# Optimization experiments

Hardware: AMD Instinct MI355X
Metric: run time of the kernel (lower is better)

The kernel has to match this reference:

```python
import jax, jax.numpy as jnp
import numpy as np

WIN = (8, 8)
N_WIN_TOK = WIN[0] * WIN[1]  # 64
DIM = 128
HEADS = 4
HEAD_DIM = DIM // HEADS
HIDDEN = int(DIM * 0.25)
B_ = 16384


def _relative_position_index():
    ch = np.arange(WIN[0])
    cw = np.arange(WIN[1])
    coords = np.stack(np.meshgrid(ch, cw, indexing='ij'))      # (2, Wh, Ww)
    flat = coords.reshape(2, -1)                                # (2, N)
    rel = flat[:, :, None] - flat[:, None, :]                   # (2, N, N)
    rel = rel.transpose(1, 2, 0).astype(np.int32)               # (N, N, 2)
    rel[:, :, 0] += WIN[0] - 1
    rel[:, :, 1] += WIN[1] - 1
    rel[:, :, 0] *= 2 * WIN[1] - 1
    return jnp.asarray(rel.sum(-1), dtype=jnp.int32)            # (N, N)


def setup_inputs() -> dict:
    key = jax.random.key(0)
    ks = jax.random.split(key, 8)
    s_in = 1.0 / np.sqrt(DIM)
    s_h = 1.0 / np.sqrt(HIDDEN)
    return {
        'x': jax.random.normal(ks[0], (B_, N_WIN_TOK, DIM), jnp.float32),
        'rpb_table': 0.02 * jax.random.normal(ks[1], ((2 * WIN[0] - 1) * (2 * WIN[1] - 1), HEADS), jnp.float32),
        'wq': s_in * jax.random.normal(ks[2], (DIM, DIM), jnp.float32),
        'bq': jnp.zeros((DIM,), jnp.float32),
        'wkv': s_in * jax.random.normal(ks[3], (DIM, 2 * DIM), jnp.float32),
        'bkv': jnp.zeros((2 * DIM,), jnp.float32),
        'fc1_w': s_in * jax.random.normal(ks[4], (DIM, HIDDEN), jnp.float32),
        'fc1_b': jnp.zeros((HIDDEN,), jnp.float32),
        'fc2_w': s_h * jax.random.normal(ks[5], (HIDDEN, DIM), jnp.float32),
        'fc2_b': jnp.zeros((DIM,), jnp.float32),
        'rel_idx': _relative_position_index(),
    }


def reference(x, rpb_table, wq, bq, wkv, bkv, fc1_w, fc1_b, fc2_w, fc2_b, rel_idx):
    B, N, C = x.shape
    scale = HEAD_DIM ** -0.5
    # qkv projections (Uformer LinearProjection): q from to_q, k/v from to_kv
    q = (x @ wq + bq).reshape(B, N, HEADS, HEAD_DIM).transpose(0, 2, 1, 3)   # (B,h,N,d)
    kv = (x @ wkv + bkv).reshape(B, N, 2, HEADS, HEAD_DIM)
    k = kv[:, :, 0].transpose(0, 2, 1, 3)                                    # (B,h,N,d)
    v = kv[:, :, 1].transpose(0, 2, 1, 3)
    attn = jnp.einsum('bhnd,bhmd->bhnm', q * scale, k)                       # (B,h,N,N)
    bias = rpb_table[rel_idx]                                                # (N,N,h)
    attn = attn + bias.transpose(2, 0, 1)[None]                              # + (1,h,N,N)
    attn = jax.nn.softmax(attn, axis=-1)
    out = jnp.einsum('bhnm,bhmd->bhnd', attn, v).transpose(0, 2, 1, 3).reshape(B, N, C)
    # Mlp proj: fc1 -> GELU -> fc2
    out = jax.nn.gelu(out @ fc1_w + fc1_b, approximate=False) @ fc2_w + fc2_b
    return out
```

## Files before the change

### kernel.cpp

```cpp
#include <hip/hip_runtime.h>
#include <hip/hip_bf16.h>
#include <math.h>

typedef __bf16 bf16x8 __attribute__((ext_vector_type(8)));
typedef __bf16 bf16x4 __attribute__((ext_vector_type(4)));
typedef float f32x4 __attribute__((ext_vector_type(4)));

static __device__ __forceinline__ f32x4 mfma16(bf16x8 a, bf16x8 b, f32x4 c) {
  return __builtin_amdgcn_mfma_f32_16x16x32_bf16(a, b, c, 0, 0, 0);
}


__global__ void wattn_prep(const float* __restrict__ wq, const float* __restrict__ bq,
                           const float* __restrict__ wkv,
                           const float* __restrict__ f1w, const float* __restrict__ f2w,
                           const float* __restrict__ rpb, const int* __restrict__ rel,
                           char* __restrict__ ws)
{
  const int idx = blockIdx.x * 256 + threadIdx.x;
  const float scale = 0.17677669529663687f;
  unsigned short* ws16 = (unsigned short*)ws;
  float* wsf = (float*)ws;

  if (idx < 2048) {
    const int lane = idx & 63, dt = (idx >> 6) & 7, kt = idx >> 9;
    const int gg = lane >> 4, cc = lane & 15;
    bf16x8 v;
#pragma unroll
    for (int i = 0; i < 8; ++i)
      v[i] = (__bf16)(wq[(kt * 32 + gg * 8 + i) * 128 + dt * 16 + cc] * scale);
    *(bf16x8*)(ws16 + idx * 8) = v;
  } else if (idx < 4096) {
    const int e = idx - 2048;
    const int lane = e & 63, dt = (e >> 6) & 7, kt = e >> 9;
    const int gg = lane >> 4, cc = lane & 15;
    bf16x8 v;
#pragma unroll
    for (int i = 0; i < 8; ++i)
      v[i] = (__bf16)(wkv[(kt * 32 + gg * 8 + i) * 256 + dt * 16 + cc]);
    *(bf16x8*)(ws16 + 16384 + e * 8) = v;
  } else if (idx < 6144) {
    const int e = idx - 4096;
    const int lane = e & 63, dt = (e >> 6) & 7, kt = e >> 9;
    const int gg = lane >> 4, cc = lane & 15;
    bf16x8 v;
#pragma unroll
    for (int i = 0; i < 8; ++i)
      v[i] = (__bf16)(wkv[(kt * 32 + gg * 8 + i) * 256 + 128 + dt * 16 + cc]);
    *(bf16x8*)(ws16 + 32768 + e * 8) = v;
  } else if (idx < 6656) {
    const int e = idx - 6144;
    const int lane = e & 63, ht = (e >> 6) & 1, kt = e >> 7;
    const int gg = lane >> 4, cc = lane & 15;
    bf16x8 v;
#pragma unroll
    for (int i = 0; i < 8; ++i)
      v[i] = (__bf16)(f1w[(kt * 32 + gg * 8 + i) * 32 + ht * 16 + cc]);
    *(bf16x8*)(ws16 + 49152 + e * 8) = v;
  } else if (idx < 7168) {
    const int e = idx - 6656;
    const int lane = e & 63, dt = e >> 6;
    const int gg = lane >> 4, cc = lane & 15;
    bf16x8 v;
#pragma unroll
    for (int i = 0; i < 8; ++i)
      v[i] = (__bf16)(f2w[(gg * 8 + i) * 128 + dt * 16 + cc]);
    *(bf16x8*)(ws16 + 53248 + e * 8) = v;
  } else if (idx < 11264) {
    const int e = idx - 7168;
    const int lane = e & 63, nt = (e >> 6) & 3, mt = (e >> 8) & 3, h = e >> 10;
    const int gg = lane >> 4, cc = lane & 15;
    const int q = nt * 16 + cc;
    f32x4 v;
#pragma unroll
    for (int r = 0; r < 4; ++r) {
      const int key = mt * 16 + gg * 4 + r;
      v[r] = rpb[rel[q * 64 + key] * 4 + h];
    }
    *(f32x4*)(wsf + 28672 + e * 4) = v;
  } else if (idx < 11392) {
    const int d = idx - 11264;
    wsf[45056 + d] = bq[d] * scale;
  }
}

__global__ __launch_bounds__(256, 3) void wattn_main(
    const float* __restrict__ x,
    const float* __restrict__ bkv,
    const float* __restrict__ f1b,
    const float* __restrict__ f2b,
    const char* __restrict__ ws,
    float* __restrict__ out)
{
  extern __shared__ char smem[];
  const int tid = threadIdx.x;
  const int w = tid >> 6;
  const int l = tid & 63;
  const int g = l >> 4;
  const int c = l & 15;
  const size_t b = blockIdx.x;
  const int WB = w * 12288;
  const int QB = WB, KB = WB + 4096, VB = WB + 8192;
  const int PB = WB, OB = WB + 8192, HB = WB;

  const unsigned short* ws16 = (const unsigned short*)ws;
  const bf16x8* wqp = (const bf16x8*)(ws16);
  const bf16x8* wkp = (const bf16x8*)(ws16 + 16384);
  const bf16x8* wvp = (const bf16x8*)(ws16 + 32768);
  const bf16x8* f1p = (const bf16x8*)(ws16 + 49152);
  const bf16x8* f2p = (const bf16x8*)(ws16 + 53248);
  const f32x4* biasp = (const f32x4*)(ws16 + 57344);
  const float* bqs = (const float*)(ws16 + 90112);

  bf16x8 xf[4][4];
  {
    const float* xg = x + b * 8192;
#pragma unroll
    for (int tt = 0; tt < 4; ++tt)
#pragma unroll
      for (int kt = 0; kt < 4; ++kt) {
        const float* p = xg + (tt * 16 + c) * 128 + kt * 32 + g * 8;
        f32x4 u = *(const f32x4*)p;
        f32x4 v = *(const f32x4*)(p + 4);
        bf16x8 f = { (__bf16)u[0], (__bf16)u[1], (__bf16)u[2], (__bf16)u[3],
                     (__bf16)v[0], (__bf16)v[1], (__bf16)v[2], (__bf16)v[3] };
        xf[tt][kt] = f;
      }
  }

#pragma unroll
  for (int dt = 0; dt < 2; ++dt) {
    const int dtg = 2 * w + dt;
    {
      f32x4 qa[4], kk[4];
      const f32x4 bq4 = *(const f32x4*)(bqs + dtg * 16 + g * 4);
      const f32x4 bk4 = *(const f32x4*)(bkv + dtg * 16 + g * 4);
#pragma unroll
      for (int tt = 0; tt < 4; ++tt) { qa[tt] = bq4; kk[tt] = bk4; }
#pragma unroll
      for (int kt = 0; kt < 4; ++kt) {
        const bf16x8 wfq = wqp[(kt * 8 + dtg) * 64 + l];
        const bf16x8 wfk = wkp[(kt * 8 + dtg) * 64 + l];
#pragma unroll
        for (int tt = 0; tt < 4; ++tt) {
          qa[tt] = mfma16(wfq, xf[tt][kt], qa[tt]);
          kk[tt] = mfma16(wfk, xf[tt][kt], kk[tt]);
        }
      }
#pragma unroll
      for (int tt = 0; tt < 4; ++tt) {
        const int q = tt * 16 + c;
        const int off = (((q >> 1) * 128 + (q & 1) * 64 + (dt * 16 + g * 4) * 2)) ^ (((q >> 1) & 7) << 4);
        bf16x4 q4 = { (__bf16)qa[tt][0], (__bf16)qa[tt][1], (__bf16)qa[tt][2], (__bf16)qa[tt][3] };
        bf16x4 k4 = { (__bf16)kk[tt][0], (__bf16)kk[tt][1], (__bf16)kk[tt][2], (__bf16)kk[tt][3] };
        *(bf16x4*)(smem + QB + off) = q4;
        *(bf16x4*)(smem + KB + off) = k4;
      }
    }
    {
      const float bv = bkv[128 + dtg * 16 + c];
      f32x4 va4[4];
#pragma unroll
      for (int tt = 0; tt < 4; ++tt) va4[tt] = (f32x4){ bv, bv, bv, bv };
#pragma unroll
      for (int kt = 0; kt < 4; ++kt) {
        const bf16x8 wf = wvp[(kt * 8 + dtg) * 64 + l];
#pragma unroll
        for (int tt = 0; tt < 4; ++tt)
          va4[tt] = mfma16(xf[tt][kt], wf, va4[tt]);
      }
#pragma unroll
      for (int tt = 0; tt < 4; ++tt) {
        const int dloc = dt * 16 + c;
        const int off = ((dloc * 128 + (tt * 16 + g * 4) * 2)) ^ ((dloc & 7) << 4);
        bf16x4 v4 = { (__bf16)va4[tt][0], (__bf16)va4[tt][1], (__bf16)va4[tt][2], (__bf16)va4[tt][3] };
        *(bf16x4*)(smem + VB + off) = v4;
      }
    }
  }

  bf16x8 ka[4], qb[4];
#pragma unroll
  for (int mt = 0; mt < 4; ++mt) {
    const int key = mt * 16 + c;
    const int off = (((key >> 1) * 128 + (key & 1) * 64 + g * 16)) ^ (((key >> 1) & 7) << 4);
    ka[mt] = *(const bf16x8*)(smem + KB + off);
  }
#pragma unroll
  for (int nt = 0; nt < 4; ++nt) {
    const int q = nt * 16 + c;
    const int off = (((q >> 1) * 128 + (q & 1) * 64 + g * 16)) ^ (((q >> 1) & 7) << 4);
    qb[nt] = *(const bf16x8*)(smem + QB + off);
  }
  f32x4 s[4][4];
#pragma unroll
  for (int mt = 0; mt < 4; ++mt)
#pragma unroll
    for (int nt = 0; nt < 4; ++nt)
      s[mt][nt] = mfma16(ka[mt], qb[nt], biasp[((w * 4 + mt) * 4 + nt) * 64 + l]);

  float rinv[4];
#pragma unroll
  for (int nt = 0; nt < 4; ++nt) {
    float m = s[0][nt][0];
#pragma unroll
    for (int mt = 0; mt < 4; ++mt)
#pragma unroll
      for (int r = 0; r < 4; ++r)
        m = fmaxf(m, s[mt][nt][r]);
    m = fmaxf(m, __shfl_xor(m, 16, 64));
    m = fmaxf(m, __shfl_xor(m, 32, 64));
    float sum = 0.f;
#pragma unroll
    for (int mt = 0; mt < 4; ++mt)
#pragma unroll
      for (int r = 0; r < 4; ++r) {
        const float e = __expf(s[mt][nt][r] - m);
        s[mt][nt][r] = e;
        sum += e;
      }
    sum += __shfl_xor(sum, 16, 64);
    sum += __shfl_xor(sum, 32, 64);
    rinv[nt] = 1.0f / sum;
  }

#pragma unroll
  for (int nt = 0; nt < 4; ++nt) {
    const int q = nt * 16 + c;
#pragma unroll
    for (int mt = 0; mt < 4; ++mt) {
      const int off = ((q * 128 + (mt * 16 + g * 4) * 2)) ^ ((q & 7) << 4);
      bf16x4 p4 = { (__bf16)s[mt][nt][0], (__bf16)s[mt][nt][1],
                    (__bf16)s[mt][nt][2], (__bf16)s[mt][nt][3] };
      *(bf16x4*)(smem + PB + off) = p4;
    }
  }

  bf16x8 va[2][2], pbf[2][4];
#pragma unroll
  for (int dt2 = 0; dt2 < 2; ++dt2)
#pragma unroll
    for (int ks = 0; ks < 2; ++ks) {
      const int dloc = dt2 * 16 + c;
      const int off = ((dloc * 128 + ks * 64 + g * 16)) ^ ((dloc & 7) << 4);
      va[dt2][ks] = *(const bf16x8*)(smem + VB + off);
    }
#pragma unroll
  for (int ks = 0; ks < 2; ++ks)
#pragma unroll
    for (int nt = 0; nt < 4; ++nt) {
      const int q = nt * 16 + c;
      const int off = ((q * 128 + ks * 64 + g * 16)) ^ ((q & 7) << 4);
      pbf[ks][nt] = *(const bf16x8*)(smem + PB + off);
    }
#pragma unroll
  for (int nt = 0; nt < 4; ++nt) {
    const float rv = rinv[nt];
    const int q = nt * 16 + c;
#pragma unroll
    for (int dt2 = 0; dt2 < 2; ++dt2) {
      f32x4 acc = { 0.f, 0.f, 0.f, 0.f };
      acc = mfma16(va[dt2][0], pbf[0][nt], acc);
      acc = mfma16(va[dt2][1], pbf[1][nt], acc);
      const int off = (((q >> 1) * 128 + (q & 1) * 64 + (dt2 * 16 + g * 4) * 2)) ^ (((q >> 1) & 7) << 4);
      bf16x4 o4 = { (__bf16)(acc[0] * rv), (__bf16)(acc[1] * rv),
                    (__bf16)(acc[2] * rv), (__bf16)(acc[3] * rv) };
      *(bf16x4*)(smem + OB + off) = o4;
    }
  }

  __syncthreads();

  bf16x8 ob[4];
#pragma unroll
  for (int kt = 0; kt < 4; ++kt) {
    const int t = w * 16 + c;
    const int off = (((t >> 1) * 128 + (t & 1) * 64 + g * 16)) ^ (((t >> 1) & 7) << 4);
    ob[kt] = *(const bf16x8*)(smem + kt * 12288 + 8192 + off);
  }
  {
#pragma unroll
    for (int ht = 0; ht < 2; ++ht) {
      f32x4 ah = *(const f32x4*)(f1b + ht * 16 + g * 4);
#pragma unroll
      for (int kt = 0; kt < 4; ++kt)
        ah = mfma16(f1p[(kt * 2 + ht) * 64 + l], ob[kt], ah);
      bf16x4 h4;
#pragma unroll
      for (int r = 0; r < 4; ++r) {
        const float v = ah[r];
        h4[r] = (__bf16)(0.5f * v * (1.0f + erff(v * 0.70710678118654752f)));
      }
      const int off = (((c >> 1) * 128 + (c & 1) * 64 + (ht * 16 + g * 4) * 2)) ^ (((c >> 1) & 7) << 4);
      *(bf16x4*)(smem + HB + off) = h4;
    }
  }
  bf16x8 ha;
  {
    const int off = (((c >> 1) * 128 + (c & 1) * 64 + g * 16)) ^ (((c >> 1) & 7) << 4);
    ha = *(const bf16x8*)(smem + HB + off);
  }
  {
    float* og = out + b * 8192 + (size_t)(w * 16) * 128;
#pragma unroll
    for (int dt = 0; dt < 8; ++dt) {
      const float bb = f2b[dt * 16 + c];
      f32x4 ay = { bb, bb, bb, bb };
      ay = mfma16(ha, f2p[dt * 64 + l], ay);
#pragma unroll
      for (int r = 0; r < 4; ++r)
        og[(g * 4 + r) * 128 + dt * 16 + c] = ay[r];
    }
  }
}

extern "C" void kernel_launch(void* const* d_in, const int* in_sizes, int n_in,
                              void* d_out, int out_size, void* d_ws, size_t ws_size,
                              hipStream_t stream) {
  const float* x    = (const float*)d_in[0];
  const float* rpb  = (const float*)d_in[1];
  const float* wq   = (const float*)d_in[2];
  const float* bq   = (const float*)d_in[3];
  const float* wkv  = (const float*)d_in[4];
  const float* bkv  = (const float*)d_in[5];
  const float* f1w  = (const float*)d_in[6];
  const float* f1b  = (const float*)d_in[7];
  const float* f2w  = (const float*)d_in[8];
  const float* f2b  = (const float*)d_in[9];
  const int*   rel  = (const int*)d_in[10];
  float* out = (float*)d_out;
  char* ws = (char*)d_ws;
  if (ws_size < 180736) return;

  const int nB = in_sizes[0] / 8192;

  wattn_prep<<<45, 256, 0, stream>>>(wq, bq, wkv, f1w, f2w, rpb, rel, ws);
  wattn_main<<<nB, 256, 49152, stream>>>(x, bkv, f1b, f2b, ws, out);
}
```

Before: 587.8 us.

## Transpose MFMA fragments in registers via ds_bpermute instead of LDS round-trips

Replaces the per-wave LDS staging of Q, K, V, P and the GELU hidden activations with in-register fragment transposes built from ds_bpermute shuffles and bf16 packing. Only the attention output still goes through a single 16 KB static LDS buffer shared by all waves before the MLP. The smaller LDS footprint allows raising launch bounds to 4 blocks per CU for more occupancy. In exchange, many bpermute instructions and select operations are added, and the higher register pressure from the packed arrays may cause spills under the tighter occupancy target.

New measurement: 587.2 us. Within noise of the previous version (-0.1%).

```diff
diff --git a/kernel.cpp b/kernel.cpp
--- a/kernel.cpp
+++ b/kernel.cpp
@@ -8,6 +8,30 @@
 
 static __device__ __forceinline__ f32x4 mfma16(bf16x8 a, bf16x8 b, f32x4 c) {
   return __builtin_amdgcn_mfma_f32_16x16x32_bf16(a, b, c, 0, 0, 0);
+}
+
+static __device__ __forceinline__ int pk2(float lo, float hi) {
+  union { __bf16 h[2]; int i; } u;
+  u.h[0] = (__bf16)lo; u.h[1] = (__bf16)hi;
+  return u.i;
+}
+
+static __device__ __forceinline__ bf16x8 xform(int aA, int aB, bool lo,
+                                               int t0a, int t0b, int t1a, int t1b) {
+  union { int d[4]; bf16x8 v; } r;
+  int x0 = __builtin_amdgcn_ds_bpermute(aA, t0a);
+  int y0 = __builtin_amdgcn_ds_bpermute(aA, t1a);
+  int x1 = __builtin_amdgcn_ds_bpermute(aA, t0b);
+  int y1 = __builtin_amdgcn_ds_bpermute(aA, t1b);
+  int x2 = __builtin_amdgcn_ds_bpermute(aB, t0a);
+  int y2 = __builtin_amdgcn_ds_bpermute(aB, t1a);
+  int x3 = __builtin_amdgcn_ds_bpermute(aB, t0b);
+  int y3 = __builtin_amdgcn_ds_bpermute(aB, t1b);
+  r.d[0] = lo ? x0 : y0;
+  r.d[1] = lo ? x1 : y1;
+  r.d[2] = lo ? x2 : y2;
+  r.d[3] = lo ? x3 : y3;
+  return r.v;
 }
 
 
@@ -84,7 +108,7 @@
   }
 }
 
-__global__ __launch_bounds__(256, 3) void wattn_main(
+__global__ __launch_bounds__(256, 4) void wattn_main(
     const float* __restrict__ x,
     const float* __restrict__ bkv,
     const float* __restrict__ f1b,
@@ -92,16 +116,16 @@
     const char* __restrict__ ws,
     float* __restrict__ out)
 {
-  extern __shared__ char smem[];
+  __shared__ __align__(16) char smem[16384];
   const int tid = threadIdx.x;
   const int w = tid >> 6;
   const int l = tid & 63;
   const int g = l >> 4;
   const int c = l & 15;
   const size_t b = blockIdx.x;
-  const int WB = w * 12288;
-  const int QB = WB, KB = WB + 4096, VB = WB + 8192;
-  const int PB = WB, OB = WB + 8192, HB = WB;
+  const int aA = ((l & 16) << 3) | ((l & 15) << 2);
+  const int aB = aA + 64;
+  const bool lolane = (l < 32);
 
   const unsigned short* ws16 = (const unsigned short*)ws;
   const bf16x8* wqp = (const bf16x8*)(ws16);
@@ -128,70 +152,82 @@
       }
   }
 
+  int qpA[2][4], qpB[2][4];
 #pragma unroll
   for (int dt = 0; dt < 2; ++dt) {
     const int dtg = 2 * w + dt;
-    {
-      f32x4 qa[4], kk[4];
-      const f32x4 bq4 = *(const f32x4*)(bqs + dtg * 16 + g * 4);
-      const f32x4 bk4 = *(const f32x4*)(bkv + dtg * 16 + g * 4);
-#pragma unroll
-      for (int tt = 0; tt < 4; ++tt) { qa[tt] = bq4; kk[tt] = bk4; }
-#pragma unroll
-      for (int kt = 0; kt < 4; ++kt) {
-        const bf16x8 wfq = wqp[(kt * 8 + dtg) * 64 + l];
-        const bf16x8 wfk = wkp[(kt * 8 + dtg) * 64 + l];
-#pragma unroll
-        for (int tt = 0; tt < 4; ++tt) {
-          qa[tt] = mfma16(wfq, xf[tt][kt], qa[tt]);
-          kk[tt] = mfma16(wfk, xf[tt][kt], kk[tt]);
-        }
-      }
-#pragma unroll
-      for (int tt = 0; tt < 4; ++tt) {
-        const int q = tt * 16 + c;
-        const int off = (((q >> 1) * 128 + (q & 1) * 64 + (dt * 16 + g * 4) * 2)) ^ (((q >> 1) & 7) << 4);
-        bf16x4 q4 = { (__bf16)qa[tt][0], (__bf16)qa[tt][1], (__bf16)qa[tt][2], (__bf16)qa[tt][3] };
-        bf16x4 k4 = { (__bf16)kk[tt][0], (__bf16)kk[tt][1], (__bf16)kk[tt][2], (__bf16)kk[tt][3] };
-        *(bf16x4*)(smem + QB + off) = q4;
-        *(bf16x4*)(smem + KB + off) = k4;
-      }
-    }
-    {
-      const float bv = bkv[128 + dtg * 16 + c];
-      f32x4 va4[4];
-#pragma unroll
-      for (int tt = 0; tt < 4; ++tt) va4[tt] = (f32x4){ bv, bv, bv, bv };
-#pragma unroll
-      for (int kt = 0; kt < 4; ++kt) {
-        const bf16x8 wf = wvp[(kt * 8 + dtg) * 64 + l];
-#pragma unroll
-        for (int tt = 0; tt < 4; ++tt)
-          va4[tt] = mfma16(xf[tt][kt], wf, va4[tt]);
-      }
-#pragma unroll
-      for (int tt = 0; tt < 4; ++tt) {
-        const int dloc = dt * 16 + c;
-        const int off = ((dloc * 128 + (tt * 16 + g * 4) * 2)) ^ ((dloc & 7) << 4);
-        bf16x4 v4 = { (__bf16)va4[tt][0], (__bf16)va4[tt][1], (__bf16)va4[tt][2], (__bf16)va4[tt][3] };
-        *(bf16x4*)(smem + VB + off) = v4;
-      }
-    }
-  }
-
-  bf16x8 ka[4], qb[4];
-#pragma unroll
-  for (int mt = 0; mt < 4; ++mt) {
-    const int key = mt * 16 + c;
-    const int off = (((key >> 1) * 128 + (key & 1) * 64 + g * 16)) ^ (((key >> 1) & 7) << 4);
-    ka[mt] = *(const bf16x8*)(smem + KB + off);
-  }
-#pragma unroll
-  for (int nt = 0; nt < 4; ++nt) {
-    const int q = nt * 16 + c;
-    const int off = (((q >> 1) * 128 + (q & 1) * 64 + g * 16)) ^ (((q >> 1) & 7) << 4);
-    qb[nt] = *(const bf16x8*)(smem + QB + off);
-  }
+    const f32x4 bq4 = *(const f32x4*)(bqs + dtg * 16 + g * 4);
+    f32x4 acc[4];
+#pragma unroll
+    for (int tt = 0; tt < 4; ++tt) acc[tt] = bq4;
+#pragma unroll
+    for (int kt = 0; kt < 4; ++kt) {
+      const bf16x8 wf = wqp[(kt * 8 + dtg) * 64 + l];
+#pragma unroll
+      for (int tt = 0; tt < 4; ++tt) acc[tt] = mfma16(wf, xf[tt][kt], acc[tt]);
+    }
+#pragma unroll
+    for (int tt = 0; tt < 4; ++tt) {
+      qpA[dt][tt] = pk2(acc[tt][0], acc[tt][1]);
+      qpB[dt][tt] = pk2(acc[tt][2], acc[tt][3]);
+    }
+  }
+  int kpA[2][4], kpB[2][4];
+#pragma unroll
+  for (int dt = 0; dt < 2; ++dt) {
+    const int dtg = 2 * w + dt;
+    const f32x4 bk4 = *(const f32x4*)(bkv + dtg * 16 + g * 4);
+    f32x4 acc[4];
+#pragma unroll
+    for (int tt = 0; tt < 4; ++tt) acc[tt] = bk4;
+#pragma unroll
+    for (int kt = 0; kt < 4; ++kt) {
+      const bf16x8 wf = wkp[(kt * 8 + dtg) * 64 + l];
+#pragma unroll
+      for (int tt = 0; tt < 4; ++tt) acc[tt] = mfma16(wf, xf[tt][kt], acc[tt]);
+    }
+#pragma unroll
+    for (int tt = 0; tt < 4; ++tt) {
+      kpA[dt][tt] = pk2(acc[tt][0], acc[tt][1]);
+      kpB[dt][tt] = pk2(acc[tt][2], acc[tt][3]);
+    }
+  }
+  bf16x8 qb[4], ka[4];
+#pragma unroll
+  for (int t4 = 0; t4 < 4; ++t4) {
+    qb[t4] = xform(aA, aB, lolane, qpA[0][t4], qpB[0][t4], qpA[1][t4], qpB[1][t4]);
+    ka[t4] = xform(aA, aB, lolane, kpA[0][t4], kpB[0][t4], kpA[1][t4], kpB[1][t4]);
+  }
+
+  int vpA[2][4], vpB[2][4];
+#pragma unroll
+  for (int dt = 0; dt < 2; ++dt) {
+    const int dtg = 2 * w + dt;
+    const float bv = bkv[128 + dtg * 16 + c];
+    f32x4 acc[4];
+#pragma unroll
+    for (int tt = 0; tt < 4; ++tt) acc[tt] = (f32x4){ bv, bv, bv, bv };
+#pragma unroll
+    for (int kt = 0; kt < 4; ++kt) {
+      const bf16x8 wf = wvp[(kt * 8 + dtg) * 64 + l];
+#pragma unroll
+      for (int tt = 0; tt < 4; ++tt) acc[tt] = mfma16(xf[tt][kt], wf, acc[tt]);
+    }
+#pragma unroll
+    for (int tt = 0; tt < 4; ++tt) {
+      vpA[dt][tt] = pk2(acc[tt][0], acc[tt][1]);
+      vpB[dt][tt] = pk2(acc[tt][2], acc[tt][3]);
+    }
+  }
+  bf16x8 va[2][2];
+#pragma unroll
+  for (int dt2 = 0; dt2 < 2; ++dt2)
+#pragma unroll
+    for (int ks = 0; ks < 2; ++ks)
+      va[dt2][ks] = xform(aA, aB, lolane,
+                          vpA[dt2][2 * ks], vpB[dt2][2 * ks],
+                          vpA[dt2][2 * ks + 1], vpB[dt2][2 * ks + 1]);
+
   f32x4 s[4][4];
 #pragma unroll
   for (int mt = 0; mt < 4; ++mt)
@@ -224,35 +260,23 @@
     rinv[nt] = 1.0f / sum;
   }
 
-#pragma unroll
-  for (int nt = 0; nt < 4; ++nt) {
-    const int q = nt * 16 + c;
-#pragma unroll
-    for (int mt = 0; mt < 4; ++mt) {
-      const int off = ((q * 128 + (mt * 16 + g * 4) * 2)) ^ ((q & 7) << 4);
-      bf16x4 p4 = { (__bf16)s[mt][nt][0], (__bf16)s[mt][nt][1],
-                    (__bf16)s[mt][nt][2], (__bf16)s[mt][nt][3] };
-      *(bf16x4*)(smem + PB + off) = p4;
-    }
-  }
-
-  bf16x8 va[2][2], pbf[2][4];
-#pragma unroll
-  for (int dt2 = 0; dt2 < 2; ++dt2)
-#pragma unroll
-    for (int ks = 0; ks < 2; ++ks) {
-      const int dloc = dt2 * 16 + c;
-      const int off = ((dloc * 128 + ks * 64 + g * 16)) ^ ((dloc & 7) << 4);
-      va[dt2][ks] = *(const bf16x8*)(smem + VB + off);
-    }
+  int ppA[4][4], ppB[4][4];
+#pragma unroll
+  for (int mt = 0; mt < 4; ++mt)
+#pragma unroll
+    for (int nt = 0; nt < 4; ++nt) {
+      ppA[mt][nt] = pk2(s[mt][nt][0], s[mt][nt][1]);
+      ppB[mt][nt] = pk2(s[mt][nt][2], s[mt][nt][3]);
+    }
+  bf16x8 pbf[2][4];
 #pragma unroll
   for (int ks = 0; ks < 2; ++ks)
 #pragma unroll
-    for (int nt = 0; nt < 4; ++nt) {
-      const int q = nt * 16 + c;
-      const int off = ((q * 128 + ks * 64 + g * 16)) ^ ((q & 7) << 4);
-      pbf[ks][nt] = *(const bf16x8*)(smem + PB + off);
-    }
+    for (int nt = 0; nt < 4; ++nt)
+      pbf[ks][nt] = xform(aA, aB, lolane,
+                          ppA[2 * ks][nt], ppB[2 * ks][nt],
+                          ppA[2 * ks + 1][nt], ppB[2 * ks + 1][nt]);
+
 #pragma unroll
   for (int nt = 0; nt < 4; ++nt) {
     const float rv = rinv[nt];
@@ -262,44 +286,44 @@
       f32x4 acc = { 0.f, 0.f, 0.f, 0.f };
       acc = mfma16(va[dt2][0], pbf[0][nt], acc);
       acc = mfma16(va[dt2][1], pbf[1][nt], acc);
-      const int off = (((q >> 1) * 128 + (q & 1) * 64 + (dt2 * 16 + g * 4) * 2)) ^ (((q >> 1) & 7) << 4);
-      bf16x4 o4 = { (__bf16)(acc[0] * rv), (__bf16)(acc[1] * rv),
-                    (__bf16)(acc[2] * rv), (__bf16)(acc[3] * rv) };
-      *(bf16x4*)(smem + OB + off) = o4;
+      const int d0 = w * 32 + dt2 * 16 + g * 4;
+      const int off = (q * 256 + d0 * 2) ^ ((q & 7) << 4);
+      union { int i[2]; bf16x4 v; } u;
+      u.i[0] = pk2(acc[0] * rv, acc[1] * rv);
+      u.i[1] = pk2(acc[2] * rv, acc[3] * rv);
+      *(bf16x4*)(smem + off) = u.v;
     }
   }
 
   __syncthreads();
 
   bf16x8 ob[4];
-#pragma unroll
-  for (int kt = 0; kt < 4; ++kt) {
+  {
     const int t = w * 16 + c;
-    const int off = (((t >> 1) * 128 + (t & 1) * 64 + g * 16)) ^ (((t >> 1) & 7) << 4);
-    ob[kt] = *(const bf16x8*)(smem + kt * 12288 + 8192 + off);
-  }
-  {
-#pragma unroll
-    for (int ht = 0; ht < 2; ++ht) {
-      f32x4 ah = *(const f32x4*)(f1b + ht * 16 + g * 4);
-#pragma unroll
-      for (int kt = 0; kt < 4; ++kt)
-        ah = mfma16(f1p[(kt * 2 + ht) * 64 + l], ob[kt], ah);
-      bf16x4 h4;
-#pragma unroll
-      for (int r = 0; r < 4; ++r) {
-        const float v = ah[r];
-        h4[r] = (__bf16)(0.5f * v * (1.0f + erff(v * 0.70710678118654752f)));
-      }
-      const int off = (((c >> 1) * 128 + (c & 1) * 64 + (ht * 16 + g * 4) * 2)) ^ (((c >> 1) & 7) << 4);
-      *(bf16x4*)(smem + HB + off) = h4;
-    }
-  }
-  bf16x8 ha;
-  {
-    const int off = (((c >> 1) * 128 + (c & 1) * 64 + g * 16)) ^ (((c >> 1) & 7) << 4);
-    ha = *(const bf16x8*)(smem + HB + off);
-  }
+#pragma unroll
+    for (int kt = 0; kt < 4; ++kt) {
+      const int off = (t * 256 + kt * 64 + g * 16) ^ ((t & 7) << 4);
+      ob[kt] = *(const bf16x8*)(smem + off);
+    }
+  }
+  int hpA[2], hpB[2];
+#pragma unroll
+  for (int ht = 0; ht < 2; ++ht) {
+    f32x4 ah = *(const f32x4*)(f1b + ht * 16 + g * 4);
+#pragma unroll
+    for (int kt = 0; kt < 4; ++kt)
+      ah = mfma16(f1p[(kt * 2 + ht) * 64 + l], ob[kt], ah);
+    float gv[4];
+#pragma unroll
+    for (int r = 0; r < 4; ++r) {
+      const float v = ah[r];
+      gv[r] = 0.5f * v * (1.0f + erff(v * 0.70710678118654752f));
+    }
+    hpA[ht] = pk2(gv[0], gv[1]);
+    hpB[ht] = pk2(gv[2], gv[3]);
+  }
+  const bf16x8 ha = xform(aA, aB, lolane, hpA[0], hpB[0], hpA[1], hpB[1]);
+
   {
     float* og = out + b * 8192 + (size_t)(w * 16) * 128;
 #pragma unroll
@@ -335,5 +359,5 @@
   const int nB = in_sizes[0] / 8192;
 
   wattn_prep<<<45, 256, 0, stream>>>(wq, bq, wkv, f1w, f2w, rpb, rel, ws);
-  wattn_main<<<nB, 256, 49152, stream>>>(x, bkv, f1b, f2b, ws, out);
-}
+  wattn_main<<<nB, 256, 0, stream>>>(x, bkv, f1b, f2b, ws, out);
+}
```
